# Optimization experiments

Hardware: AMD Instinct MI355X
Metric: run time of the kernel (lower is better)

Reference implementation:

```python
import jax, jax.numpy as jnp
import numpy as np
from jax import lax

THRESH = 0.8
LENS = 0.4
DECAY = 0.2
LOG_SIG_MIN, LOG_SIG_MAX = -20.0, 2.0
WINS = 15

@jax.custom_vjp
def act_fun(x):
    return (x > THRESH).astype(x.dtype)

def _act_fwd(x):
    return act_fun(x), x

def _act_bwd(x, g):
    return (g * (jnp.abs(x - THRESH) < LENS).astype(g.dtype),)

act_fun.defvjp(_act_fwd, _act_bwd)

B, NIN, HID, NACT = 2048, 512, 1024, 32

def _xavier(key, out_d, in_d):
    lim = jnp.sqrt(6.0 / (in_d + out_d)).astype(jnp.float32)
    return jax.random.uniform(key, (out_d, in_d), jnp.float32, -lim, lim)

def setup_inputs() -> dict:
    key = jax.random.key(0)
    ks = jax.random.split(key, 12)
    inp = {
        'state': jax.random.normal(ks[0], (B, 5, NIN), jnp.float32),
        'w1': _xavier(ks[1], HID, NIN), 'b1': jnp.zeros((HID,), jnp.float32),
        'w2': _xavier(ks[2], HID, NIN), 'b2': jnp.zeros((HID,), jnp.float32),
        'w3': _xavier(ks[3], HID, NIN), 'b3': jnp.zeros((HID,), jnp.float32),
        'wl': _xavier(ks[4], 1, 3), 'bl': jnp.zeros((1,), jnp.float32),
        'w11': _xavier(ks[5], HID, 4 * HID), 'b11': jnp.zeros((HID,), jnp.float32),
        'w12': _xavier(ks[6], HID, HID), 'b12': jnp.zeros((HID,), jnp.float32),
        'w21': _xavier(ks[7], HID, 4 * HID), 'b21': jnp.zeros((HID,), jnp.float32),
        'w22': _xavier(ks[8], HID, HID), 'b22': jnp.zeros((HID,), jnp.float32),
        'wm': _xavier(ks[9], NACT, HID), 'bm': jnp.zeros((NACT,), jnp.float32),
        'ws': _xavier(ks[10], NACT, HID), 'bs': jnp.zeros((NACT,), jnp.float32),
    }
    return inp

def _policy_forward(state, w1, b1, w2, b2, w3, b3, wl, bl,
                    w11, b11, w12, b12, w21, b21, w22, b22, wm, bm, ws, bs):
    batch = state.shape[0]
    hid = w1.shape[0]
    seq = jnp.repeat(state, 3, axis=1)
    mem0 = jnp.zeros((batch, hid, 4), state.dtype)
    sp0 = jnp.zeros((batch, hid, 4), state.dtype)

    def step(carry, x_t):
        mem, spike = carry
        i1 = x_t @ w1.T + b1  # [B, HID]
        i2 = x_t @ w2.T + b2
        i3 = x_t @ w3.T + b3
        inner = jnp.einsum('bck,k->bc', mem[:, :, :3], wl[0]) + bl[0]
        inp_all = jnp.stack([i1, i2, i3, inner], axis=-1)  # [B, HID, 4]
        mem1 = mem * DECAY * (1.0 - spike) + inp_all
        sp1 = act_fun(mem1)
        return (mem1, sp1), sp1

    _, spikes = lax.scan(step, (mem0, sp0), jnp.swapaxes(seq, 0, 1))  # [T,B,HID,4]
    spikes = jnp.transpose(spikes, (1, 0, 2, 3)).reshape(batch, WINS, hid * 4)
    x = jnp.mean(spikes, axis=1)  # [B, 4*HID]

    x1 = jax.nn.relu(x @ w11.T + b11)
    x1 = jax.nn.relu(x1 @ w12.T + b12)
    mean = x1 @ wm.T + bm

    x2 = jax.nn.relu(x @ w21.T + b21)
    x2 = jax.nn.relu(x2 @ w22.T + b22)
    log_std = jnp.clip(x2 @ ws.T + bs, LOG_SIG_MIN, LOG_SIG_MAX)
    return mean, log_std

def reference(state, w1, b1, w2, b2, w3, b3, wl, bl,
              w11, b11, w12, b12, w21, b21, w22, b22, wm, bm, ws, bs):
    return _policy_forward(state, w1, b1, w2, b2, w3, b3, wl, bl,
                           w11, b11, w12, b12, w21, b21, w22, b22, wm, bm, ws, bs)
```

## Files before the change

### kernel.cpp

```cpp
#include <hip/hip_runtime.h>
#include <cstddef>
#include <cstdint>

#define THRESH 0.8f
#define DECAY  0.2f

typedef unsigned short ushort_t;
typedef __attribute__((ext_vector_type(8))) short bf16x8;
typedef __attribute__((ext_vector_type(4))) float f32x4;
typedef __attribute__((ext_vector_type(4))) int i32x4;

__device__ __forceinline__ ushort_t f2bf(float f) {
    union { float f; unsigned u; } v; v.f = f;
    unsigned r = v.u + 0x7FFFu + ((v.u >> 16) & 1u);
    return (ushort_t)(r >> 16);
}
__device__ __forceinline__ float bf2f(ushort_t h) {
    union { unsigned u; float f; } v; v.u = ((unsigned)h) << 16;
    return v.f;
}
__device__ __forceinline__ float blo(unsigned u) {
    union { unsigned x; float f; } v; v.x = u << 16; return v.f;
}
__device__ __forceinline__ float bhi(unsigned u) {
    union { unsigned x; float f; } v; v.x = u & 0xFFFF0000u; return v.f;
}

__device__ __forceinline__ void gload16(const void* g, void* l) {
    __builtin_amdgcn_global_load_lds(
        (const __attribute__((address_space(1))) void*)g,
        (__attribute__((address_space(3))) void*)l,
        16, 0, 0);
}

#define DSREAD(dst, addr, off) \
    asm volatile("ds_read_b128 %0, %1 offset:" #off : "=v"(dst) : "v"(addr))

#define MM(i, j, a, w) \
    acc[i][j] = __builtin_amdgcn_mfma_f32_16x16x32_bf16(a, w, acc[i][j], 0, 0, 0)

__global__ __launch_bounds__(512, 4) void fused_cur_lif(
    const ushort_t* __restrict__ A, const ushort_t* __restrict__ W,
    const float* __restrict__ b123, const float* __restrict__ wl,
    const float* __restrict__ bl, signed char* __restrict__ xb)
{
    __shared__ ushort_t lds[3][11264];

    const int t = threadIdx.x;
    const int bx = blockIdx.x;
    const int by = blockIdx.y;
    const int lane = t & 63;
    const int wv = t >> 6;
    const int wm = (wv >> 2) * 80;
    const int wn = (wv & 3) * 48;
    const int fr = lane & 15;
    const int fq = lane >> 4;
    const int swz16 = (fq ^ ((fr >> 1) & 3)) * 16;

    const unsigned av0 = (unsigned)((wm + fr) * 64 + swz16);
    const unsigned av1 = av0 + 22528;
    const unsigned av2 = av0 + 45056;
    const unsigned bv0 = (unsigned)(10240 + (wn + fr) * 64 + swz16);
    const unsigned bv1 = bv0 + 22528;
    const unsigned bv2 = bv0 + 45056;

    const ushort_t* src0; const ushort_t* src1;
    const ushort_t* src2; const ushort_t* src3;
    int dst0, dst1, dst2, dst3;
    if (wv < 5) {
        const int rl0 = wv * 32 + (lane >> 2);
        const int rl1 = rl0 + 16;
        src0 = A + (size_t)(bx * 160 + rl0) * 1536 + ((lane & 3) ^ ((rl0 >> 1) & 3)) * 8;
        src1 = A + (size_t)(bx * 160 + rl1) * 1536 + ((lane & 3) ^ ((rl1 >> 1) & 3)) * 8;
        src2 = src0; src3 = src1;
        dst0 = rl0 * 32 + (lane & 3) * 8;
        dst1 = rl1 * 32 + (lane & 3) * 8;
        dst2 = dst0; dst3 = dst1;
    } else {
        const int rb = (wv - 5) * 64 + (lane >> 2);
        src0 = W + (size_t)(by * 192 + rb) * 1536 + ((lane & 3) ^ ((rb >> 1) & 3)) * 8;
        src1 = src0 + (size_t)16 * 1536;
        src2 = src0 + (size_t)32 * 1536;
        src3 = src0 + (size_t)48 * 1536;
        dst0 = 5120 + rb * 32 + (lane & 3) * 8;
        dst1 = dst0 + 16 * 32;
        dst2 = dst0 + 32 * 32;
        dst3 = dst0 + 48 * 32;
    }

#define STAGE(tile, sbuf)                                              \
    do {                                                               \
        ushort_t* lb_ = &lds[sbuf][0];                                 \
        if (wv < 5) {                                                  \
            gload16(src0 + (tile) * 32, lb_ + dst0);                   \
            gload16(src1 + (tile) * 32, lb_ + dst1);                   \
        } else {                                                       \
            gload16(src0 + (tile) * 32, lb_ + dst0);                   \
            gload16(src1 + (tile) * 32, lb_ + dst1);                   \
            gload16(src2 + (tile) * 32, lb_ + dst2);                   \
            gload16(src3 + (tile) * 32, lb_ + dst3);                   \
        }                                                              \
    } while (0)

#define COMPUTE(av_, bv_)                                              \
    do {                                                               \
        bf16x8 af0, af1, af2, af3, af4, wf0, wf1, wf2;                 \
        DSREAD(af0, av_, 0);                                           \
        DSREAD(af1, av_, 1024);                                        \
        DSREAD(af2, av_, 2048);                                        \
        DSREAD(af3, av_, 3072);                                        \
        DSREAD(af4, av_, 4096);                                        \
        DSREAD(wf0, bv_, 0);                                           \
        DSREAD(wf1, bv_, 1024);                                        \
        DSREAD(wf2, bv_, 2048);                                        \
        asm volatile("s_waitcnt lgkmcnt(0)" ::: "memory");             \
        __builtin_amdgcn_sched_barrier(0);                             \
        __builtin_amdgcn_s_setprio(1);                                 \
        MM(0, 0, af0, wf0); MM(0, 1, af0, wf1); MM(0, 2, af0, wf2);    \
        MM(1, 0, af1, wf0); MM(1, 1, af1, wf1); MM(1, 2, af1, wf2);    \
        MM(2, 0, af2, wf0); MM(2, 1, af2, wf1); MM(2, 2, af2, wf2);    \
        MM(3, 0, af3, wf0); MM(3, 1, af3, wf1); MM(3, 2, af3, wf2);    \
        MM(4, 0, af4, wf0); MM(4, 1, af4, wf1); MM(4, 2, af4, wf2);    \
        __builtin_amdgcn_s_setprio(0);                                 \
    } while (0)

    f32x4 acc[5][3];
#pragma unroll
    for (int i = 0; i < 5; i++)
#pragma unroll
        for (int j = 0; j < 3; j++) {
            f32x4 z = {0.f, 0.f, 0.f, 0.f};
            acc[i][j] = z;
        }

    STAGE(0, 0);
    STAGE(1, 1);

#pragma unroll
    for (int tt = 0; tt < 46; ++tt) {
        STAGE(tt + 2, (tt + 2) % 3);
        if (wv < 5) asm volatile("s_waitcnt vmcnt(4)" ::: "memory");
        else        asm volatile("s_waitcnt vmcnt(8)" ::: "memory");
        __builtin_amdgcn_s_barrier();
        __builtin_amdgcn_sched_barrier(0);
        const unsigned av_ = (tt % 3 == 0) ? av0 : (tt % 3 == 1) ? av1 : av2;
        const unsigned bv_ = (tt % 3 == 0) ? bv0 : (tt % 3 == 1) ? bv1 : bv2;
        COMPUTE(av_, bv_);
        __builtin_amdgcn_s_barrier();
        __builtin_amdgcn_sched_barrier(0);
    }
    if (wv < 5) asm volatile("s_waitcnt vmcnt(2)" ::: "memory");
    else        asm volatile("s_waitcnt vmcnt(4)" ::: "memory");
    __builtin_amdgcn_s_barrier();
    __builtin_amdgcn_sched_barrier(0);
    COMPUTE(av1, bv1);
    __builtin_amdgcn_s_barrier();
    __builtin_amdgcn_sched_barrier(0);
    asm volatile("s_waitcnt vmcnt(0)" ::: "memory");
    __builtin_amdgcn_s_barrier();
    __builtin_amdgcn_sched_barrier(0);
    COMPUTE(av2, bv2);
#undef STAGE
#undef COMPUTE

    const int ch = by * 64 + (wv & 3) * 16 + fr;
    const float b1c = b123[ch];
    const float b2c = b123[1024 + ch];
    const float b3c = b123[2048 + ch];
    const float wl0 = wl[0], wl1 = wl[1], wl2 = wl[2], bl0 = bl[0];
    const int bbase = bx * 32 + (wv >> 2) * 16 + fq * 4;
#pragma unroll
    for (int r = 0; r < 4; r++) {
        float m0 = 0.f, m1 = 0.f, m2 = 0.f, m3 = 0.f;
        int s0 = 0, s1 = 0, s2 = 0, s3 = 0;
#pragma unroll
        for (int f = 0; f < 5; f++) {
            const float i1 = acc[f][0][r] + b1c;
            const float i2 = acc[f][1][r] + b2c;
            const float i3 = acc[f][2][r] + b3c;
#pragma unroll
            for (int rep = 0; rep < 3; rep++) {
                const float inner = m0 * wl0 + m1 * wl1 + m2 * wl2 + bl0;
                const float n0 = i1 + ((m0 > THRESH) ? 0.f : DECAY * m0);
                const float n1 = i2 + ((m1 > THRESH) ? 0.f : DECAY * m1);
                const float n2 = i3 + ((m2 > THRESH) ? 0.f : DECAY * m2);
                const float n3 = inner + ((m3 > THRESH) ? 0.f : DECAY * m3);
                m0 = n0; m1 = n1; m2 = n2; m3 = n3;
                s0 += (n0 > THRESH); s1 += (n1 > THRESH);
                s2 += (n2 > THRESH); s3 += (n3 > THRESH);
            }
        }
        uchar4 o;
        o.x = (unsigned char)s0; o.y = (unsigned char)s1;
        o.z = (unsigned char)s2; o.w = (unsigned char)s3;
        *(uchar4*)&xb[(size_t)(bbase + r) * 4096 + ch * 4] = o;
    }
}

__global__ __launch_bounds__(256) void mlp1_i8(
    const signed char* __restrict__ A, const signed char* __restrict__ W,
    const float* __restrict__ wsc, const float* __restrict__ bias,
    ushort_t* __restrict__ C)
{
    __shared__ signed char sA[64 * 64];
    __shared__ signed char sW[128 * 64];

    const int t = threadIdx.x;
    const int mBase = blockIdx.x * 64;
    const int nBase = blockIdx.y * 128;

    const int lane = t & 63;
    const int wv = t >> 6;
    const int wn = wv * 32;
    const int fr = lane & 15;
    const int fq = lane >> 4;
    const int fsw = (fq ^ ((fr >> 1) & 3)) * 16;

    const int r0 = t >> 2;
    const int cc = ((t & 3) ^ ((t >> 3) & 3)) * 16;

    i32x4 acc[4][2];
#pragma unroll
    for (int i = 0; i < 4; i++)
#pragma unroll
        for (int j = 0; j < 2; j++) {
            i32x4 z = {0, 0, 0, 0};
            acc[i][j] = z;
        }

    for (int k0 = 0; k0 < 4096; k0 += 64) {
        gload16(&A[(size_t)(mBase + r0) * 4096 + k0 + cc], &sA[t * 16]);
        gload16(&W[(size_t)(nBase + r0) * 4096 + k0 + cc], &sW[t * 16]);
        gload16(&W[(size_t)(nBase + 64 + r0) * 4096 + k0 + cc], &sW[4096 + t * 16]);
        __syncthreads();

        i32x4 af[4], wf[2];
#pragma unroll
        for (int i = 0; i < 4; i++)
            af[i] = *(const i32x4*)&sA[(i * 16 + fr) * 64 + fsw];
#pragma unroll
        for (int j = 0; j < 2; j++)
            wf[j] = *(const i32x4*)&sW[(wn + j * 16 + fr) * 64 + fsw];
#pragma unroll
        for (int i = 0; i < 4; i++)
#pragma unroll
            for (int j = 0; j < 2; j++)
                acc[i][j] = __builtin_amdgcn_mfma_i32_16x16x64_i8(af[i], wf[j], acc[i][j], 0, 0, 0);
        __syncthreads();
    }

#pragma unroll
    for (int j = 0; j < 2; j++) {
        const int col = nBase + wn + j * 16 + fr;
        const float sc = wsc[col];
        const float bv = bias[col];
#pragma unroll
        for (int i = 0; i < 4; i++)
#pragma unroll
            for (int r = 0; r < 4; r++) {
                const int row = mBase + i * 16 + fq * 4 + r;
                const float v = (float)acc[i][j][r] * sc + bv;
                C[(size_t)row * 2048 + col] = f2bf(fmaxf(v, 0.f));
            }
    }
}

__global__ __launch_bounds__(256) void mlp2_bf16(
    const ushort_t* __restrict__ A, const ushort_t* __restrict__ W,
    const float* __restrict__ bias, ushort_t* __restrict__ C,
    int N, int K, int lda, int ldw, int ldc, int aHalfOff)
{
    __shared__ ushort_t sA[64 * 32];
    __shared__ ushort_t sW[128 * 32];

    const int t = threadIdx.x;
    const int mBase = blockIdx.x * 64;
    const int nBase = blockIdx.y * 128;
    const int aOff = (2 * nBase >= N) ? aHalfOff : 0;

    const int lane = t & 63;
    const int wv = t >> 6;
    const int wn = wv * 32;
    const int fr = lane & 15;
    const int fq = lane >> 4;
    const int fsw = (fq ^ ((fr >> 1) & 3)) * 8;

    const int r0 = t >> 2;
    const int cc = ((t & 3) ^ ((t >> 3) & 3)) * 8;

    f32x4 acc[4][2];
#pragma unroll
    for (int i = 0; i < 4; i++)
#pragma unroll
        for (int j = 0; j < 2; j++) {
            f32x4 z = {0.f, 0.f, 0.f, 0.f};
            acc[i][j] = z;
        }

    for (int k0 = 0; k0 < K; k0 += 32) {
        gload16(&A[(size_t)(mBase + r0) * lda + aOff + k0 + cc], &sA[t * 8]);
        gload16(&W[(size_t)(nBase + r0) * ldw + k0 + cc], &sW[t * 8]);
        gload16(&W[(size_t)(nBase + 64 + r0) * ldw + k0 + cc], &sW[2048 + t * 8]);
        __syncthreads();

        bf16x8 af[4], wf[2];
#pragma unroll
        for (int i = 0; i < 4; i++)
            af[i] = *(const bf16x8*)&sA[(i * 16 + fr) * 32 + fsw];
#pragma unroll
        for (int j = 0; j < 2; j++)
            wf[j] = *(const bf16x8*)&sW[(wn + j * 16 + fr) * 32 + fsw];
#pragma unroll
        for (int i = 0; i < 4; i++)
#pragma unroll
            for (int j = 0; j < 2; j++)
                acc[i][j] = __builtin_amdgcn_mfma_f32_16x16x32_bf16(af[i], wf[j], acc[i][j], 0, 0, 0);
        __syncthreads();
    }

#pragma unroll
    for (int j = 0; j < 2; j++) {
        const int col = nBase + wn + j * 16 + fr;
        const float bv = bias[col];
#pragma unroll
        for (int i = 0; i < 4; i++)
#pragma unroll
            for (int r = 0; r < 4; r++) {
                const int row = mBase + i * 16 + fq * 4 + r;
                C[(size_t)row * ldc + col] = f2bf(fmaxf(acc[i][j][r] + bv, 0.f));
            }
    }
}

__device__ __forceinline__ void split_state_perm(const float4* src, ushort4* dst,
                                                 int base, int t) {
#pragma unroll
    for (int p = 0; p < 4; p++) {
        const int i = base * 1024 + p * 256 + t;
        const float4 v = src[i];
        ushort4 h, l;
        h.x = f2bf(v.x); l.x = f2bf(v.x - bf2f(h.x));
        h.y = f2bf(v.y); l.y = f2bf(v.y - bf2f(h.y));
        h.z = f2bf(v.z); l.z = f2bf(v.z - bf2f(h.z));
        h.w = f2bf(v.w); l.w = f2bf(v.w - bf2f(h.w));
        const int s = i >> 7, c4 = i & 127;
        const int b = s / 5, f = s - b * 5;
        const int m = ((b >> 5) * 160) + (((b >> 4) & 1) * 80) + (f << 4) + (b & 15);
        ushort4* row = dst + (size_t)m * 384;
        row[c4] = h; row[128 + c4] = h; row[256 + c4] = l;
    }
}
__device__ __forceinline__ void split_w_perm(const float4* src, ushort4* dst,
                                             int base, int t, int j) {
#pragma unroll
    for (int p = 0; p < 4; p++) {
        const int i = base * 1024 + p * 256 + t;
        const float4 v = src[i];
        ushort4 h, l;
        h.x = f2bf(v.x); l.x = f2bf(v.x - bf2f(h.x));
        h.y = f2bf(v.y); l.y = f2bf(v.y - bf2f(h.y));
        h.z = f2bf(v.z); l.z = f2bf(v.z - bf2f(h.z));
        h.w = f2bf(v.w); l.w = f2bf(v.w - bf2f(h.w));
        const int c = i >> 7, c4 = i & 127;
        const int n = ((c >> 6) * 192) + (((c >> 4) & 3) * 48) + (j << 4) + (c & 15);
        ushort4* row = dst + (size_t)n * 384;
        row[c4] = h; row[128 + c4] = l; row[256 + c4] = h;
    }
}
__device__ __forceinline__ void do_cvt4(const float4* src, ushort4* dst,
                                        int base, int t) {
#pragma unroll
    for (int p = 0; p < 4; p++) {
        const int i = base * 1024 + p * 256 + t;
        const float4 v = src[i];
        ushort4 h;
        h.x = f2bf(v.x); h.y = f2bf(v.y); h.z = f2bf(v.z); h.w = f2bf(v.w);
        dst[i] = h;
    }
}
__device__ __forceinline__ int q8(float x, float inv) {
    int q = (int)rintf(x * inv);
    q = q > 127 ? 127 : (q < -127 ? -127 : q);
    return q & 0xff;
}

__global__ __launch_bounds__(256) void prep_kernel(
    const float* __restrict__ state,
    const float* __restrict__ w1, const float* __restrict__ w2,
    const float* __restrict__ w3,
    const float* __restrict__ w11, const float* __restrict__ w21,
    const float* __restrict__ w12, const float* __restrict__ w22,
    const float* __restrict__ b1, const float* __restrict__ b2,
    const float* __restrict__ b3, const float* __restrict__ b11,
    const float* __restrict__ b21, const float* __restrict__ b12,
    const float* __restrict__ b22,
    ushort_t* __restrict__ Ap, ushort_t* __restrict__ Wp,
    signed char* __restrict__ w1q, float* __restrict__ wsc,
    ushort_t* __restrict__ w2b,
    float* __restrict__ b123, float* __restrict__ bb1, float* __restrict__ bb2)
{
    const int bid = blockIdx.x;
    const int t = threadIdx.x;
    if (bid < 1280) {
        split_state_perm((const float4*)state, (ushort4*)Ap, bid, t);
    } else if (bid < 1408) {
        split_w_perm((const float4*)w1, (ushort4*)Wp, bid - 1280, t, 0);
    } else if (bid < 1536) {
        split_w_perm((const float4*)w2, (ushort4*)Wp, bid - 1408, t, 1);
    } else if (bid < 1664) {
        split_w_perm((const float4*)w3, (ushort4*)Wp, bid - 1536, t, 2);
    } else if (bid < 3712) {
        const int r = bid - 1664;
        const float* src = (r < 1024) ? (w11 + (size_t)r * 4096)
                                      : (w21 + (size_t)(r - 1024) * 4096);
        __shared__ float red[256];
        float4 v[4];
        float lmax = 0.f;
#pragma unroll
        for (int p = 0; p < 4; p++) {
            v[p] = ((const float4*)src)[t * 4 + p];
            lmax = fmaxf(lmax, fmaxf(fmaxf(fabsf(v[p].x), fabsf(v[p].y)),
                                     fmaxf(fabsf(v[p].z), fabsf(v[p].w))));
        }
        red[t] = lmax;
        __syncthreads();
        for (int s = 128; s > 0; s >>= 1) {
            if (t < s) red[t] = fmaxf(red[t], red[t + s]);
            __syncthreads();
        }
        const float gmax = fmaxf(red[0], 1e-30f);
        const float inv = 127.0f / gmax;
        int4 o;
        o.x = q8(v[0].x, inv) | (q8(v[0].y, inv) << 8) | (q8(v[0].z, inv) << 16) | (q8(v[0].w, inv) << 24);
        o.y = q8(v[1].x, inv) | (q8(v[1].y, inv) << 8) | (q8(v[1].z, inv) << 16) | (q8(v[1].w, inv) << 24);
        o.z = q8(v[2].x, inv) | (q8(v[2].y, inv) << 8) | (q8(v[2].z, inv) << 16) | (q8(v[2].w, inv) << 24);
        o.w = q8(v[3].x, inv) | (q8(v[3].y, inv) << 8) | (q8(v[3].z, inv) << 16) | (q8(v[3].w, inv) << 24);
        ((int4*)(w1q + (size_t)r * 4096))[t] = o;
        if (t == 0) wsc[r] = gmax / (127.0f * 15.0f);
    } else if (bid < 3968) {
        do_cvt4((const float4*)w12, (ushort4*)w2b, bid - 3712, t);
    } else if (bid < 4224) {
        do_cvt4((const float4*)w22, (ushort4*)(w2b + 1048576), bid - 3968, t);
    } else {
#pragma unroll
        for (int p = 0; p < 4; p++) {
            const int i = p * 256 + t;
            b123[i] = b1[i]; b123[1024 + i] = b2[i]; b123[2048 + i] = b3[i];
            bb1[i] = b11[i]; bb1[1024 + i] = b21[i];
            bb2[i] = b12[i]; bb2[1024 + i] = b22[i];
        }
    }
}

__global__ __launch_bounds__(256) void head_kernel(
    const ushort_t* __restrict__ h, const float* __restrict__ wm,
    const float* __restrict__ bm, const float* __restrict__ ws,
    const float* __restrict__ bs, float* __restrict__ out)
{
    const int t = threadIdx.x;
    const int branch = blockIdx.x >> 8;
    const int n = t & 31;
    const int b = (blockIdx.x & 255) * 8 + (t >> 5);
    const ushort_t* hr = h + (size_t)b * 2048 + branch * 1024;
    const float* wr = (branch ? ws : wm) + (size_t)n * 1024;
    float s = 0.f;
#pragma unroll 4
    for (int k = 0; k < 1024; k += 8) {
        const uint4 hv = *(const uint4*)&hr[k];
        const float4 w0 = *(const float4*)&wr[k];
        const float4 w1 = *(const float4*)&wr[k + 4];
        s += blo(hv.x) * w0.x + bhi(hv.x) * w0.y
           + blo(hv.y) * w0.z + bhi(hv.y) * w0.w
           + blo(hv.z) * w1.x + bhi(hv.z) * w1.y
           + blo(hv.w) * w1.z + bhi(hv.w) * w1.w;
    }
    s += (branch ? bs : bm)[n];
    if (branch) s = fminf(fmaxf(s, -20.f), 2.f);
    out[(size_t)branch * 65536 + (size_t)b * 32 + n] = s;
}

extern "C" void kernel_launch(void* const* d_in, const int* in_sizes, int n_in,
                              void* d_out, int out_size, void* d_ws, size_t ws_size,
                              hipStream_t stream)
{
    const float* state = (const float*)d_in[0];
    const float* w1  = (const float*)d_in[1];  const float* b1  = (const float*)d_in[2];
    const float* w2  = (const float*)d_in[3];  const float* b2  = (const float*)d_in[4];
    const float* w3  = (const float*)d_in[5];  const float* b3  = (const float*)d_in[6];
    const float* wl  = (const float*)d_in[7];  const float* bl  = (const float*)d_in[8];
    const float* w11 = (const float*)d_in[9];  const float* b11 = (const float*)d_in[10];
    const float* w12 = (const float*)d_in[11]; const float* b12 = (const float*)d_in[12];
    const float* w21 = (const float*)d_in[13]; const float* b21 = (const float*)d_in[14];
    const float* w22 = (const float*)d_in[15]; const float* b22 = (const float*)d_in[16];
    const float* wm  = (const float*)d_in[17]; const float* bm  = (const float*)d_in[18];
    const float* ws  = (const float*)d_in[19]; const float* bs  = (const float*)d_in[20];
    float* out = (float*)d_out;

    char* wp = (char*)d_ws;
    ushort_t*    Ap    = (ushort_t*)wp;    wp += (size_t)10240 * 1536 * 2;
    ushort_t*    Wp    = (ushort_t*)wp;    wp += (size_t)3072 * 1536 * 2;
    signed char* xb    = (signed char*)wp; wp += (size_t)2048 * 4096;
    signed char* w1q   = (signed char*)wp; wp += (size_t)2048 * 4096;
    ushort_t*    w2b   = (ushort_t*)wp;    wp += (size_t)2048 * 1024 * 2;
    ushort_t*    h1    = (ushort_t*)wp;    wp += (size_t)2048 * 2048 * 2;
    ushort_t*    h2    = (ushort_t*)wp;    wp += (size_t)2048 * 2048 * 2;
    float*       wsc   = (float*)wp;       wp += 2048 * 4;
    float*       b123  = (float*)wp;       wp += 3072 * 4;
    float*       bb1   = (float*)wp;       wp += 2048 * 4;
    float*       bb2   = (float*)wp;       wp += 2048 * 4;

    prep_kernel<<<4225, 256, 0, stream>>>(
        state, w1, w2, w3, w11, w21, w12, w22,
        b1, b2, b3, b11, b21, b12, b22,
        Ap, Wp, w1q, wsc, w2b, b123, bb1, bb2);

    fused_cur_lif<<<dim3(64, 16), 512, 0, stream>>>(Ap, Wp, b123, wl, bl, xb);

    mlp1_i8<<<dim3(32, 16), 256, 0, stream>>>(xb, w1q, wsc, bb1, h1);

    mlp2_bf16<<<dim3(32, 16), 256, 0, stream>>>(
        h1, w2b, bb2, h2, 2048, 1024, 2048, 1024, 2048, 1024);

    head_kernel<<<512, 256, 0, stream>>>(h2, wm, bm, ws, bs, out);
}
```

Before: 365.1 us.

## Shrink split-bf16 operands, remap blocks per XCD, overlap LDS reads, shuffle reduction

The split-bf16 A and W buffers drop their duplicated hi segment, going from 1536 to 1024 columns per row. The GEMM keeps three K passes (hi*hi, hi*lo, lo*hi) by remapping tile offsets through atile/wtile. This cuts prep writes and GEMM global loads by about a third. The launch becomes a 1D grid remapped so each XCD handles contiguous W column blocks for L2 reuse. LDS reads are reordered so the first MFMA row starts after a partial lgkmcnt wait, and the w1 quantization max-reduction uses wave shuffles instead of a log-step shared-memory tree.

```diff
diff --git a/kernel.cpp b/kernel.cpp
--- a/kernel.cpp
+++ b/kernel.cpp
@@ -38,6 +38,13 @@
 
 #define MM(i, j, a, w) \
     acc[i][j] = __builtin_amdgcn_mfma_f32_16x16x32_bf16(a, w, acc[i][j], 0, 0, 0)
+
+__device__ __forceinline__ constexpr int atile(int t) {
+    return t < 16 ? t * 32 : (t < 32 ? (t - 16) * 32 : 512 + (t - 32) * 32);
+}
+__device__ __forceinline__ constexpr int wtile(int t) {
+    return t < 16 ? t * 32 : (t < 32 ? 512 + (t - 16) * 32 : (t - 32) * 32);
+}
 
 __global__ __launch_bounds__(512, 4) void fused_cur_lif(
     const ushort_t* __restrict__ A, const ushort_t* __restrict__ W,
@@ -47,8 +54,11 @@
     __shared__ ushort_t lds[3][11264];
 
     const int t = threadIdx.x;
-    const int bx = blockIdx.x;
-    const int by = blockIdx.y;
+    const int bid = blockIdx.x;
+    const int xcd = bid & 7;
+    const int idx = bid >> 3;
+    const int by = xcd * 2 + (idx >> 6);
+    const int bx = idx & 63;
     const int lane = t & 63;
     const int wv = t >> 6;
     const int wm = (wv >> 2) * 80;
@@ -70,18 +80,18 @@
     if (wv < 5) {
         const int rl0 = wv * 32 + (lane >> 2);
         const int rl1 = rl0 + 16;
-        src0 = A + (size_t)(bx * 160 + rl0) * 1536 + ((lane & 3) ^ ((rl0 >> 1) & 3)) * 8;
-        src1 = A + (size_t)(bx * 160 + rl1) * 1536 + ((lane & 3) ^ ((rl1 >> 1) & 3)) * 8;
+        src0 = A + (size_t)(bx * 160 + rl0) * 1024 + ((lane & 3) ^ ((rl0 >> 1) & 3)) * 8;
+        src1 = A + (size_t)(bx * 160 + rl1) * 1024 + ((lane & 3) ^ ((rl1 >> 1) & 3)) * 8;
         src2 = src0; src3 = src1;
         dst0 = rl0 * 32 + (lane & 3) * 8;
         dst1 = rl1 * 32 + (lane & 3) * 8;
         dst2 = dst0; dst3 = dst1;
     } else {
         const int rb = (wv - 5) * 64 + (lane >> 2);
-        src0 = W + (size_t)(by * 192 + rb) * 1536 + ((lane & 3) ^ ((rb >> 1) & 3)) * 8;
-        src1 = src0 + (size_t)16 * 1536;
-        src2 = src0 + (size_t)32 * 1536;
-        src3 = src0 + (size_t)48 * 1536;
+        src0 = W + (size_t)(by * 192 + rb) * 1024 + ((lane & 3) ^ ((rb >> 1) & 3)) * 8;
+        src1 = src0 + (size_t)16 * 1024;
+        src2 = src0 + (size_t)32 * 1024;
+        src3 = src0 + (size_t)48 * 1024;
         dst0 = 5120 + rb * 32 + (lane & 3) * 8;
         dst1 = dst0 + 16 * 32;
         dst2 = dst0 + 32 * 32;
@@ -92,13 +102,13 @@
     do {                                                               \
         ushort_t* lb_ = &lds[sbuf][0];                                 \
         if (wv < 5) {                                                  \
-            gload16(src0 + (tile) * 32, lb_ + dst0);                   \
-            gload16(src1 + (tile) * 32, lb_ + dst1);                   \
+            gload16(src0 + atile(tile), lb_ + dst0);                   \
+            gload16(src1 + atile(tile), lb_ + dst1);                   \
         } else {                                                       \
-            gload16(src0 + (tile) * 32, lb_ + dst0);                   \
-            gload16(src1 + (tile) * 32, lb_ + dst1);                   \
-            gload16(src2 + (tile) * 32, lb_ + dst2);                   \
-            gload16(src3 + (tile) * 32, lb_ + dst3);                   \
+            gload16(src0 + wtile(tile), lb_ + dst0);                   \
+            gload16(src1 + wtile(tile), lb_ + dst1);                   \
+            gload16(src2 + wtile(tile), lb_ + dst2);                   \
+            gload16(src3 + wtile(tile), lb_ + dst3);                   \
         }                                                              \
     } while (0)
 
@@ -106,17 +116,19 @@
     do {                                                               \
         bf16x8 af0, af1, af2, af3, af4, wf0, wf1, wf2;                 \
         DSREAD(af0, av_, 0);                                           \
+        DSREAD(wf0, bv_, 0);                                           \
+        DSREAD(wf1, bv_, 1024);                                        \
+        DSREAD(wf2, bv_, 2048);                                        \
         DSREAD(af1, av_, 1024);                                        \
         DSREAD(af2, av_, 2048);                                        \
         DSREAD(af3, av_, 3072);                                        \
         DSREAD(af4, av_, 4096);                                        \
-        DSREAD(wf0, bv_, 0);                                           \
-        DSREAD(wf1, bv_, 1024);                                        \
-        DSREAD(wf2, bv_, 2048);                                        \
-        asm volatile("s_waitcnt lgkmcnt(0)" ::: "memory");             \
+        asm volatile("s_waitcnt lgkmcnt(4)" ::: "memory");             \
         __builtin_amdgcn_sched_barrier(0);                             \
         __builtin_amdgcn_s_setprio(1);                                 \
         MM(0, 0, af0, wf0); MM(0, 1, af0, wf1); MM(0, 2, af0, wf2);    \
+        asm volatile("s_waitcnt lgkmcnt(0)" ::: "memory");             \
+        __builtin_amdgcn_sched_barrier(0);                             \
         MM(1, 0, af1, wf0); MM(1, 1, af1, wf1); MM(1, 2, af1, wf2);    \
         MM(2, 0, af2, wf0); MM(2, 1, af2, wf1); MM(2, 2, af2, wf2);    \
         MM(3, 0, af3, wf0); MM(3, 1, af3, wf1); MM(3, 2, af3, wf2);    \
@@ -346,8 +358,8 @@
         const int s = i >> 7, c4 = i & 127;
         const int b = s / 5, f = s - b * 5;
         const int m = ((b >> 5) * 160) + (((b >> 4) & 1) * 80) + (f << 4) + (b & 15);
-        ushort4* row = dst + (size_t)m * 384;
-        row[c4] = h; row[128 + c4] = h; row[256 + c4] = l;
+        ushort4* row = dst + (size_t)m * 256;
+        row[c4] = h; row[128 + c4] = l;
     }
 }
 __device__ __forceinline__ void split_w_perm(const float4* src, ushort4* dst,
@@ -363,8 +375,8 @@
         h.w = f2bf(v.w); l.w = f2bf(v.w - bf2f(h.w));
         const int c = i >> 7, c4 = i & 127;
         const int n = ((c >> 6) * 192) + (((c >> 4) & 3) * 48) + (j << 4) + (c & 15);
-        ushort4* row = dst + (size_t)n * 384;
-        row[c4] = h; row[128 + c4] = l; row[256 + c4] = h;
+        ushort4* row = dst + (size_t)n * 256;
+        row[c4] = h; row[128 + c4] = l;
     }
 }
 __device__ __forceinline__ void do_cvt4(const float4* src, ushort4* dst,
@@ -413,7 +425,7 @@
         const int r = bid - 1664;
         const float* src = (r < 1024) ? (w11 + (size_t)r * 4096)
                                       : (w21 + (size_t)(r - 1024) * 4096);
-        __shared__ float red[256];
+        __shared__ float red4[4];
         float4 v[4];
         float lmax = 0.f;
 #pragma unroll
@@ -422,13 +434,13 @@
             lmax = fmaxf(lmax, fmaxf(fmaxf(fabsf(v[p].x), fabsf(v[p].y)),
                                      fmaxf(fabsf(v[p].z), fabsf(v[p].w))));
         }
-        red[t] = lmax;
+#pragma unroll
+        for (int d = 1; d < 64; d <<= 1)
+            lmax = fmaxf(lmax, __shfl_xor(lmax, d, 64));
+        if ((t & 63) == 0) red4[t >> 6] = lmax;
         __syncthreads();
-        for (int s = 128; s > 0; s >>= 1) {
-            if (t < s) red[t] = fmaxf(red[t], red[t + s]);
-            __syncthreads();
-        }
-        const float gmax = fmaxf(red[0], 1e-30f);
+        const float gmax = fmaxf(fmaxf(fmaxf(red4[0], red4[1]),
+                                       fmaxf(red4[2], red4[3])), 1e-30f);
         const float inv = 127.0f / gmax;
         int4 o;
         o.x = q8(v[0].x, inv) | (q8(v[0].y, inv) << 8) | (q8(v[0].z, inv) << 16) | (q8(v[0].w, inv) << 24);
@@ -497,8 +509,8 @@
     float* out = (float*)d_out;
 
     char* wp = (char*)d_ws;
-    ushort_t*    Ap    = (ushort_t*)wp;    wp += (size_t)10240 * 1536 * 2;
-    ushort_t*    Wp    = (ushort_t*)wp;    wp += (size_t)3072 * 1536 * 2;
+    ushort_t*    Ap    = (ushort_t*)wp;    wp += (size_t)10240 * 1024 * 2;
+    ushort_t*    Wp    = (ushort_t*)wp;    wp += (size_t)3072 * 1024 * 2;
     signed char* xb    = (signed char*)wp; wp += (size_t)2048 * 4096;
     signed char* w1q   = (signed char*)wp; wp += (size_t)2048 * 4096;
     ushort_t*    w2b   = (ushort_t*)wp;    wp += (size_t)2048 * 1024 * 2;
@@ -514,7 +526,7 @@
         b1, b2, b3, b11, b21, b12, b22,
         Ap, Wp, w1q, wsc, w2b, b123, bb1, bb2);
 
-    fused_cur_lif<<<dim3(64, 16), 512, 0, stream>>>(Ap, Wp, b123, wl, bl, xb);
+    fused_cur_lif<<<1024, 512, 0, stream>>>(Ap, Wp, b123, wl, bl, xb);
 
     mlp1_i8<<<dim3(32, 16), 256, 0, stream>>>(xb, w1q, wsc, bb1, h1);
 
```

Result: slower. 399.5 us (+9.4%).
